# Performance work log

Measured on AMD Instinct MI355X. Metric: run time of the kernel, lower is better.

## Reference

```python
import jax, jax.numpy as jnp
import numpy as np

B, N, E, M, H, OUT, F = 4, 10000, 160000, 4, 64, 64, 64


def setup_inputs() -> dict:
    key = jax.random.key(0)
    k1, k2, k3, k4, k5, k6 = jax.random.split(key, 6)
    node_fts = jax.random.normal(k1, (B, N, M, H), dtype=jnp.float32)
    hidden = jax.random.normal(k2, (B, N, M, H), dtype=jnp.float32)
    edge_fts = jax.random.normal(k3, (B, E, F), dtype=jnp.float32)
    edge_indices = jax.random.randint(k4, (B, E, 2), 0, N, dtype=jnp.int64)
    # hk.Linear params (truncated-normal-ish init approximated by scaled normal)
    W_nh = jax.random.normal(k5, (2 * H, OUT), dtype=jnp.float32) / np.sqrt(2 * H)
    b_nh = jnp.zeros((OUT,), dtype=jnp.float32)
    W_e = jax.random.normal(k6, (F, 1), dtype=jnp.float32) / np.sqrt(F)
    b_e = jnp.zeros((1,), dtype=jnp.float32)
    return {"node_fts": node_fts, "hidden": hidden, "edge_fts": edge_fts,
            "W_nh": W_nh, "b_nh": b_nh, "W_e": W_e, "b_e": b_e,
            "edge_indices": edge_indices}


def reference(node_fts, hidden, edge_fts, W_nh, b_nh, W_e, b_e, edge_indices):
    nb_nodes = node_fts.shape[1]
    src = edge_indices[..., 0]  # [B, E]
    tgt = edge_indices[..., 1]  # [B, E]
    # fuse node and hidden features, project: [B, N, M, 2H] @ [2H, OUT]
    nh = jnp.concatenate([node_fts, hidden], axis=-1)
    nh_fts = jnp.einsum('bnmc,co->bnmo', nh, W_nh) + b_nh  # [B, N, M, OUT]
    # gather per-edge source-node features along node axis
    nh_values = jnp.take_along_axis(nh_fts, src[:, :, None, None], axis=1)  # [B, E, M, OUT]
    # scalar gate per edge
    edge_coeff = jnp.einsum('bef,fo->beo', edge_fts, W_e) + b_e  # [B, E, 1]
    filtered = edge_coeff[..., None] * nh_values  # [B, E, M, OUT]
    # scatter-sum messages to target nodes, per batch element
    seg = jax.vmap(lambda d, s: jax.ops.segment_sum(d, s, num_segments=nb_nodes))
    updated_bits = seg(filtered, tgt)  # [B, N, M, OUT]
    return updated_bits
```

## Files before the change

### kernel.cpp

```cpp
#include <hip/hip_runtime.h>

#define Bc 4
#define Nc 10000
#define Ec 160000
#define Mc 4
#define Hc 64
#define OUTc 64
#define Fc 64
#define ROWS (Bc * Nc * Mc)
#define TILES (ROWS / 16)
#define NSEG (Bc * Nc)
#define NEDGE (Bc * Ec)
#define PROJ_BLOCKS 2500
#define GATE_BLOCKS 2500
#define CAP 64

typedef __attribute__((ext_vector_type(8))) short bf16x8;
typedef __attribute__((ext_vector_type(4))) float f32x4;

__device__ __forceinline__ unsigned short f2bf(float f) {
    union { float f; unsigned u; } x; x.f = f;
    return (unsigned short)((x.u + 0x7FFFu + ((x.u >> 16) & 1u)) >> 16);
}
__device__ __forceinline__ float bfhi(unsigned u) {
    union { unsigned u; float f; } x; x.u = u & 0xFFFF0000u; return x.f;
}
__device__ __forceinline__ float bflo(unsigned u) {
    union { unsigned u; float f; } x; x.u = u << 16; return x.f;
}

__global__ __launch_bounds__(256) void proj_gate_kernel(
    const float* __restrict__ node, const float* __restrict__ hid,
    const float* __restrict__ Wnh, const float* __restrict__ bnh,
    unsigned short* __restrict__ nhf,
    const float* __restrict__ efts, const int* __restrict__ eidx,
    const float* __restrict__ We, const float* __restrict__ be,
    int2* __restrict__ epair, int* __restrict__ cnt)
{
    __shared__ __align__(16) unsigned short wlds[8192];
    const int lane = threadIdx.x & 63;

    if (blockIdx.x < PROJ_BLOCKS) {
        const int t = threadIdx.x;
#pragma unroll
        for (int i = 0; i < 4; ++i) {
            const int f    = t + 256 * i;
            const int kt   = f >> 8;
            const int ct   = (f >> 6) & 3;
            const int l    = f & 63;
            const int quad = l >> 4, m = l & 15;
            const int col  = 16 * ct + m;
            const int krow = quad * 8 + 32 * kt;
            bf16x8 fr;
#pragma unroll
            for (int j = 0; j < 8; ++j)
                fr[j] = (short)f2bf(Wnh[(size_t)(krow + j) * 64 + col]);
            *(bf16x8*)(wlds + (size_t)f * 8) = fr;
        }
        __syncthreads();

        const int tile = (int)(blockIdx.x * 4 + (threadIdx.x >> 6));
        const int m    = lane & 15;
        const int quad = lane >> 4;

        float bias[4];
#pragma unroll
        for (int ct = 0; ct < 4; ++ct) bias[ct] = bnh[m + 16 * ct];

        const int arow = tile * 16 + m;
        f32x4 acc[4];
#pragma unroll
        for (int ct = 0; ct < 4; ++ct) acc[ct] = (f32x4){0.f, 0.f, 0.f, 0.f};

#pragma unroll
        for (int kt = 0; kt < 4; ++kt) {
            const int kbase = quad * 8 + 32 * kt;
            const float* p = (kbase < 64)
                ? (node + (size_t)arow * 64 + kbase)
                : (hid  + (size_t)arow * 64 + (kbase - 64));
            const float4 lo = *(const float4*)p;
            const float4 hi = *(const float4*)(p + 4);
            bf16x8 a;
            a[0] = (short)f2bf(lo.x); a[1] = (short)f2bf(lo.y);
            a[2] = (short)f2bf(lo.z); a[3] = (short)f2bf(lo.w);
            a[4] = (short)f2bf(hi.x); a[5] = (short)f2bf(hi.y);
            a[6] = (short)f2bf(hi.z); a[7] = (short)f2bf(hi.w);
#pragma unroll
            for (int ct = 0; ct < 4; ++ct) {
                const bf16x8 bf = *(const bf16x8*)(wlds + (size_t)((kt * 4 + ct) * 64 + lane) * 8);
                acc[ct] = __builtin_amdgcn_mfma_f32_16x16x32_bf16(a, bf, acc[ct], 0, 0, 0);
            }
        }

        const int r0 = tile * 16 + quad * 4;
#pragma unroll
        for (int ct = 0; ct < 4; ++ct) {
            const int col = m + 16 * ct;
#pragma unroll
            for (int reg = 0; reg < 4; ++reg)
                nhf[(size_t)(r0 + reg) * 64 + col] = f2bf(acc[ct][reg] + bias[ct]);
        }
    } else {
        const int w  = (int)((blockIdx.x - PROJ_BLOCKS) * 4 + (threadIdx.x >> 6));
        const int e0 = w * 64;
        if (e0 >= NEDGE) return;
        const int b = e0 / Ec;

        const float4 w4 = *(const float4*)(We + (size_t)(lane & 15) * 4);
        const float* base = efts + (size_t)e0 * 64;
        float p[16];
#pragma unroll
        for (int j = 0; j < 16; ++j) {
            const float4 v = *(const float4*)(base + (size_t)j * 256 + lane * 4);
            p[j] = v.x * w4.x + v.y * w4.y + v.z * w4.z + v.w * w4.w;
        }
#pragma unroll
        for (int off = 1, n = 8; off < 16; off <<= 1, n >>= 1) {
            const bool hi = (lane & off) != 0;
#pragma unroll
            for (int i = 0; i < 8; ++i) {
                if (i < n) {
                    const float keep = hi ? p[2 * i + 1] : p[2 * i];
                    const float send = hi ? p[2 * i] : p[2 * i + 1];
                    p[i] = keep + __shfl_xor(send, off, 64);
                }
            }
        }
        const float c = p[0] + be[0];

        const int el = e0 + 4 * (lane & 15) + (lane >> 4);
        const int2 st = *(const int2*)(eidx + (size_t)el * 2);
        const int seg  = b * Nc + st.y;
        const int slot = atomicAdd(&cnt[seg], 1);
        if (slot < CAP)
            epair[(size_t)seg * 128 + slot] = make_int2(st.x, __float_as_int(c));
    }
}

__global__ __launch_bounds__(256) void gather_kernel(
    const int* __restrict__ cnt, const int2* epair,
    const unsigned* __restrict__ nhf, float* out)
{
    const int lane = threadIdx.x & 63;
    int seg = (int)((blockIdx.x * blockDim.x + threadIdx.x) >> 6);
    if (seg >= NSEG) return;
    seg = __builtin_amdgcn_readfirstlane(seg);
    const int b = seg / Nc;
    const int deg = cnt[seg];
    const int end = deg < CAP ? deg : CAP;
    const int2* bp = epair + (size_t)seg * 128;
    const unsigned* base = nhf + (size_t)b * Nc * 128 + lane * 2;

    f32x4 acc[4];
#pragma unroll
    for (int j = 0; j < 4; ++j) acc[j] = (f32x4){0.f, 0.f, 0.f, 0.f};

    int i = 0;
    for (; i + 8 <= end; i += 8) {
        int2 p[8]; uint2 r[8];
#pragma unroll
        for (int j = 0; j < 8; ++j) p[j] = bp[i + j];
#pragma unroll
        for (int j = 0; j < 8; ++j) r[j] = *(const uint2*)(base + (size_t)p[j].x * 128);
#pragma unroll
        for (int j = 0; j < 8; ++j) {
            const float c = __int_as_float(p[j].y);
            acc[j & 3][0] += c * bflo(r[j].x);
            acc[j & 3][1] += c * bfhi(r[j].x);
            acc[j & 3][2] += c * bflo(r[j].y);
            acc[j & 3][3] += c * bfhi(r[j].y);
        }
    }
    if (i + 4 <= end) {
        int2 p[4]; uint2 r[4];
#pragma unroll
        for (int j = 0; j < 4; ++j) p[j] = bp[i + j];
#pragma unroll
        for (int j = 0; j < 4; ++j) r[j] = *(const uint2*)(base + (size_t)p[j].x * 128);
#pragma unroll
        for (int j = 0; j < 4; ++j) {
            const float c = __int_as_float(p[j].y);
            acc[j][0] += c * bflo(r[j].x);
            acc[j][1] += c * bfhi(r[j].x);
            acc[j][2] += c * bflo(r[j].y);
            acc[j][3] += c * bfhi(r[j].y);
        }
        i += 4;
    }
    for (; i < end; ++i) {
        const int2 p = bp[i];
        const uint2 r = *(const uint2*)(base + (size_t)p.x * 128);
        const float c = __int_as_float(p.y);
        acc[0][0] += c * bflo(r.x);
        acc[0][1] += c * bfhi(r.x);
        acc[0][2] += c * bflo(r.y);
        acc[0][3] += c * bfhi(r.y);
    }
    float4 o;
    o.x = (acc[0][0] + acc[1][0]) + (acc[2][0] + acc[3][0]);
    o.y = (acc[0][1] + acc[1][1]) + (acc[2][1] + acc[3][1]);
    o.z = (acc[0][2] + acc[1][2]) + (acc[2][2] + acc[3][2]);
    o.w = (acc[0][3] + acc[1][3]) + (acc[2][3] + acc[3][3]);
    *(float4*)(out + (size_t)seg * 256 + lane * 4) = o;
}

__global__ __launch_bounds__(256) void edge_atomic_kernel(
    const float* __restrict__ efts, const int* __restrict__ eidx,
    const float* __restrict__ We, const float* __restrict__ be,
    const unsigned* __restrict__ nhf, float* __restrict__ out)
{
    const int lane = threadIdx.x & 63;
    const int eg   = (int)((blockIdx.x * blockDim.x + threadIdx.x) >> 6);
    if (eg >= NEDGE) return;
    const int b = eg / Ec;
    float c = efts[(size_t)eg * 64 + lane] * We[lane];
#pragma unroll
    for (int off = 32; off > 0; off >>= 1) c += __shfl_xor(c, off, 64);
    c += be[0];
    const int src = eidx[(size_t)eg * 2 + 0];
    const int tgt = eidx[(size_t)eg * 2 + 1];
    const uint2 r = *(const uint2*)(nhf + ((size_t)(b * Nc + src)) * 128 + lane * 2);
    float* op = out + ((size_t)(b * Nc + tgt)) * 256 + lane * 4;
    atomicAdd(op + 0, c * bflo(r.x));
    atomicAdd(op + 1, c * bfhi(r.x));
    atomicAdd(op + 2, c * bflo(r.y));
    atomicAdd(op + 3, c * bfhi(r.y));
}

extern "C" void kernel_launch(void* const* d_in, const int* in_sizes, int n_in,
                              void* d_out, int out_size, void* d_ws, size_t ws_size,
                              hipStream_t stream) {
    const float* node = (const float*)d_in[0];
    const float* hid  = (const float*)d_in[1];
    const float* efts = (const float*)d_in[2];
    const float* Wnh  = (const float*)d_in[3];
    const float* bnh  = (const float*)d_in[4];
    const float* We   = (const float*)d_in[5];
    const float* be   = (const float*)d_in[6];
    const int*   eidx = (const int*)d_in[7];
    float* out = (float*)d_out;

    unsigned* ws = (unsigned*)d_ws;
    unsigned short* nhf16 = (unsigned short*)ws;
    int* cnt = (int*)(ws + 5120000);
    const size_t ws_needed = (size_t)5160000 * 4;

    if (ws_size >= ws_needed) {
        int2* epair = (int2*)d_out;
        hipMemsetAsync(cnt, 0, (size_t)NSEG * sizeof(int), stream);
        proj_gate_kernel<<<PROJ_BLOCKS + GATE_BLOCKS, 256, 0, stream>>>(
            node, hid, Wnh, bnh, nhf16, efts, eidx, We, be, epair, cnt);
        gather_kernel<<<NSEG / 4, 256, 0, stream>>>(cnt, epair, (const unsigned*)ws, out);
    } else {
        proj_gate_kernel<<<PROJ_BLOCKS, 256, 0, stream>>>(
            node, hid, Wnh, bnh, nhf16, efts, eidx, We, be,
            (int2*)d_out , (int*)d_out );
        hipMemsetAsync(d_out, 0, (size_t)out_size * sizeof(float), stream);
        edge_atomic_kernel<<<NEDGE / 4, 256, 0, stream>>>(efts, eidx, We, be, (const unsigned*)ws, out);
    }
}
```

Measured before the change: 345.6 us.

## Split fused proj/gate kernel, double work per wave, broadcast edge pairs via shuffles

Splits the fused projection+gate kernel into separate proj and gate kernels. Each wave now handles two 16-row tiles (proj) or 128 edges (gate), with all loads issued before the math so memory latency overlaps compute. The gather kernel loads the segment's edge pairs once per lane and broadcasts them with shuffles instead of re-reading them from memory. The cost is an extra kernel launch, the loss of concurrency between projection and gate work, and higher register pressure.

Measured after the change: 351.9 us. About the same (+1.8%).

```diff
diff --git a/kernel.cpp b/kernel.cpp
--- a/kernel.cpp
+++ b/kernel.cpp
@@ -3,17 +3,11 @@
 #define Bc 4
 #define Nc 10000
 #define Ec 160000
-#define Mc 4
-#define Hc 64
-#define OUTc 64
-#define Fc 64
-#define ROWS (Bc * Nc * Mc)
-#define TILES (ROWS / 16)
 #define NSEG (Bc * Nc)
 #define NEDGE (Bc * Ec)
-#define PROJ_BLOCKS 2500
-#define GATE_BLOCKS 2500
 #define CAP 64
+#define PROJ_BLOCKS 1250
+#define GATE_BLOCKS 1250
 
 typedef __attribute__((ext_vector_type(8))) short bf16x8;
 typedef __attribute__((ext_vector_type(4))) float f32x4;
@@ -29,70 +23,89 @@
     union { unsigned u; float f; } x; x.u = u << 16; return x.f;
 }
 
-__global__ __launch_bounds__(256) void proj_gate_kernel(
+__device__ __forceinline__ float reduce16(float* p, int lane) {
+#pragma unroll
+    for (int off = 1, n = 8; off < 16; off <<= 1, n >>= 1) {
+        const bool hi2 = (lane & off) != 0;
+#pragma unroll
+        for (int i = 0; i < 8; ++i)
+            if (i < n) {
+                const float keep = hi2 ? p[2 * i + 1] : p[2 * i];
+                const float send = hi2 ? p[2 * i] : p[2 * i + 1];
+                p[i] = keep + __shfl_xor(send, off, 64);
+            }
+    }
+    return p[0];
+}
+
+__global__ __launch_bounds__(256) void proj_kernel(
     const float* __restrict__ node, const float* __restrict__ hid,
     const float* __restrict__ Wnh, const float* __restrict__ bnh,
-    unsigned short* __restrict__ nhf,
-    const float* __restrict__ efts, const int* __restrict__ eidx,
-    const float* __restrict__ We, const float* __restrict__ be,
-    int2* __restrict__ epair, int* __restrict__ cnt)
+    unsigned short* __restrict__ nhf)
 {
     __shared__ __align__(16) unsigned short wlds[8192];
-    const int lane = threadIdx.x & 63;
-
-    if (blockIdx.x < PROJ_BLOCKS) {
-        const int t = threadIdx.x;
-#pragma unroll
-        for (int i = 0; i < 4; ++i) {
-            const int f    = t + 256 * i;
-            const int kt   = f >> 8;
-            const int ct   = (f >> 6) & 3;
-            const int l    = f & 63;
-            const int quad = l >> 4, m = l & 15;
-            const int col  = 16 * ct + m;
-            const int krow = quad * 8 + 32 * kt;
-            bf16x8 fr;
-#pragma unroll
-            for (int j = 0; j < 8; ++j)
-                fr[j] = (short)f2bf(Wnh[(size_t)(krow + j) * 64 + col]);
-            *(bf16x8*)(wlds + (size_t)f * 8) = fr;
-        }
-        __syncthreads();
-
-        const int tile = (int)(blockIdx.x * 4 + (threadIdx.x >> 6));
-        const int m    = lane & 15;
-        const int quad = lane >> 4;
-
-        float bias[4];
-#pragma unroll
-        for (int ct = 0; ct < 4; ++ct) bias[ct] = bnh[m + 16 * ct];
-
-        const int arow = tile * 16 + m;
-        f32x4 acc[4];
-#pragma unroll
-        for (int ct = 0; ct < 4; ++ct) acc[ct] = (f32x4){0.f, 0.f, 0.f, 0.f};
-
+    const int t = threadIdx.x;
+    const int lane = t & 63;
+
+#pragma unroll
+    for (int i = 0; i < 4; ++i) {
+        const int f    = t + 256 * i;
+        const int kt   = f >> 8;
+        const int ct   = (f >> 6) & 3;
+        const int l    = f & 63;
+        const int quad = l >> 4, m = l & 15;
+        const int col  = 16 * ct + m;
+        const int krow = quad * 8 + 32 * kt;
+        bf16x8 fr;
+#pragma unroll
+        for (int j = 0; j < 8; ++j)
+            fr[j] = (short)f2bf(Wnh[(size_t)(krow + j) * 64 + col]);
+        *(bf16x8*)(wlds + (size_t)f * 8) = fr;
+    }
+    __syncthreads();
+
+    const int wv   = (int)(blockIdx.x * 4 + (t >> 6));
+    const int m    = lane & 15;
+    const int quad = lane >> 4;
+
+    float bias[4];
+#pragma unroll
+    for (int ct = 0; ct < 4; ++ct) bias[ct] = bnh[m + 16 * ct];
+
+    float4 lo[2][4], hi[2][4];
+#pragma unroll
+    for (int half = 0; half < 2; ++half) {
+        const int arow = (wv * 2 + half) * 16 + m;
 #pragma unroll
         for (int kt = 0; kt < 4; ++kt) {
             const int kbase = quad * 8 + 32 * kt;
-            const float* p = (kbase < 64)
+            const float* pp = (kbase < 64)
                 ? (node + (size_t)arow * 64 + kbase)
                 : (hid  + (size_t)arow * 64 + (kbase - 64));
-            const float4 lo = *(const float4*)p;
-            const float4 hi = *(const float4*)(p + 4);
+            lo[half][kt] = *(const float4*)pp;
+            hi[half][kt] = *(const float4*)(pp + 4);
+        }
+    }
+
+#pragma unroll
+    for (int half = 0; half < 2; ++half) {
+        f32x4 acc[4];
+#pragma unroll
+        for (int ct = 0; ct < 4; ++ct) acc[ct] = (f32x4){0.f, 0.f, 0.f, 0.f};
+#pragma unroll
+        for (int kt = 0; kt < 4; ++kt) {
             bf16x8 a;
-            a[0] = (short)f2bf(lo.x); a[1] = (short)f2bf(lo.y);
-            a[2] = (short)f2bf(lo.z); a[3] = (short)f2bf(lo.w);
-            a[4] = (short)f2bf(hi.x); a[5] = (short)f2bf(hi.y);
-            a[6] = (short)f2bf(hi.z); a[7] = (short)f2bf(hi.w);
+            a[0] = (short)f2bf(lo[half][kt].x); a[1] = (short)f2bf(lo[half][kt].y);
+            a[2] = (short)f2bf(lo[half][kt].z); a[3] = (short)f2bf(lo[half][kt].w);
+            a[4] = (short)f2bf(hi[half][kt].x); a[5] = (short)f2bf(hi[half][kt].y);
+            a[6] = (short)f2bf(hi[half][kt].z); a[7] = (short)f2bf(hi[half][kt].w);
 #pragma unroll
             for (int ct = 0; ct < 4; ++ct) {
                 const bf16x8 bf = *(const bf16x8*)(wlds + (size_t)((kt * 4 + ct) * 64 + lane) * 8);
                 acc[ct] = __builtin_amdgcn_mfma_f32_16x16x32_bf16(a, bf, acc[ct], 0, 0, 0);
             }
         }
-
-        const int r0 = tile * 16 + quad * 4;
+        const int r0 = (wv * 2 + half) * 16 + quad * 4;
 #pragma unroll
         for (int ct = 0; ct < 4; ++ct) {
             const int col = m + 16 * ct;
@@ -100,40 +113,59 @@
             for (int reg = 0; reg < 4; ++reg)
                 nhf[(size_t)(r0 + reg) * 64 + col] = f2bf(acc[ct][reg] + bias[ct]);
         }
-    } else {
-        const int w  = (int)((blockIdx.x - PROJ_BLOCKS) * 4 + (threadIdx.x >> 6));
-        const int e0 = w * 64;
-        if (e0 >= NEDGE) return;
-        const int b = e0 / Ec;
-
-        const float4 w4 = *(const float4*)(We + (size_t)(lane & 15) * 4);
-        const float* base = efts + (size_t)e0 * 64;
-        float p[16];
-#pragma unroll
-        for (int j = 0; j < 16; ++j) {
-            const float4 v = *(const float4*)(base + (size_t)j * 256 + lane * 4);
-            p[j] = v.x * w4.x + v.y * w4.y + v.z * w4.z + v.w * w4.w;
-        }
-#pragma unroll
-        for (int off = 1, n = 8; off < 16; off <<= 1, n >>= 1) {
-            const bool hi = (lane & off) != 0;
-#pragma unroll
-            for (int i = 0; i < 8; ++i) {
-                if (i < n) {
-                    const float keep = hi ? p[2 * i + 1] : p[2 * i];
-                    const float send = hi ? p[2 * i] : p[2 * i + 1];
-                    p[i] = keep + __shfl_xor(send, off, 64);
-                }
-            }
-        }
-        const float c = p[0] + be[0];
-
-        const int el = e0 + 4 * (lane & 15) + (lane >> 4);
-        const int2 st = *(const int2*)(eidx + (size_t)el * 2);
-        const int seg  = b * Nc + st.y;
+    }
+}
+
+__global__ __launch_bounds__(256) void gate_kernel(
+    const float* __restrict__ efts, const int* __restrict__ eidx,
+    const float* __restrict__ We, const float* __restrict__ be,
+    int2* __restrict__ epair, int* __restrict__ cnt)
+{
+    const int lane = threadIdx.x & 63;
+    const int w  = (int)(blockIdx.x * 4 + (threadIdx.x >> 6));
+    const int e0 = w * 128;
+    const int b  = e0 / Ec;
+    const int cb = b * Nc;
+    const float4 w4 = *(const float4*)(We + (size_t)(lane & 15) * 4);
+    const float be0 = be[0];
+    const int perm = 4 * (lane & 15) + (lane >> 4);
+
+    float4 v[16];
+    const float* base0 = efts + (size_t)e0 * 64;
+#pragma unroll
+    for (int j = 0; j < 16; ++j)
+        v[j] = *(const float4*)(base0 + (size_t)j * 256 + lane * 4);
+    const int2 st0 = *(const int2*)(eidx + (size_t)(e0 + perm) * 2);
+
+    float p[16];
+#pragma unroll
+    for (int j = 0; j < 16; ++j)
+        p[j] = v[j].x * w4.x + v[j].y * w4.y + v[j].z * w4.z + v[j].w * w4.w;
+
+    const float* base1 = efts + (size_t)(e0 + 64) * 64;
+#pragma unroll
+    for (int j = 0; j < 16; ++j)
+        v[j] = *(const float4*)(base1 + (size_t)j * 256 + lane * 4);
+    const int2 st1 = *(const int2*)(eidx + (size_t)(e0 + 64 + perm) * 2);
+
+    {
+        const float cval = reduce16(p, lane) + be0;
+        const int seg  = cb + st0.y;
         const int slot = atomicAdd(&cnt[seg], 1);
         if (slot < CAP)
-            epair[(size_t)seg * 128 + slot] = make_int2(st.x, __float_as_int(c));
+            epair[(size_t)seg * 128 + slot] = make_int2(st0.x, __float_as_int(cval));
+    }
+
+#pragma unroll
+    for (int j = 0; j < 16; ++j)
+        p[j] = v[j].x * w4.x + v[j].y * w4.y + v[j].z * w4.z + v[j].w * w4.w;
+
+    {
+        const float cval = reduce16(p, lane) + be0;
+        const int seg  = cb + st1.y;
+        const int slot = atomicAdd(&cnt[seg], 1);
+        if (slot < CAP)
+            epair[(size_t)seg * 128 + slot] = make_int2(st1.x, __float_as_int(cval));
     }
 }
 
@@ -150,6 +182,7 @@
     const int end = deg < CAP ? deg : CAP;
     const int2* bp = epair + (size_t)seg * 128;
     const unsigned* base = nhf + (size_t)b * Nc * 128 + lane * 2;
+    const int2 my = bp[lane];
 
     f32x4 acc[4];
 #pragma unroll
@@ -157,44 +190,48 @@
 
     int i = 0;
     for (; i + 8 <= end; i += 8) {
-        int2 p[8]; uint2 r[8];
-#pragma unroll
-        for (int j = 0; j < 8; ++j) p[j] = bp[i + j];
-#pragma unroll
-        for (int j = 0; j < 8; ++j) r[j] = *(const uint2*)(base + (size_t)p[j].x * 128);
+        int sx[8]; float cc[8]; uint2 r[8];
 #pragma unroll
         for (int j = 0; j < 8; ++j) {
-            const float c = __int_as_float(p[j].y);
-            acc[j & 3][0] += c * bflo(r[j].x);
-            acc[j & 3][1] += c * bfhi(r[j].x);
-            acc[j & 3][2] += c * bflo(r[j].y);
-            acc[j & 3][3] += c * bfhi(r[j].y);
+            sx[j] = __shfl(my.x, i + j, 64);
+            cc[j] = __int_as_float(__shfl(my.y, i + j, 64));
+        }
+#pragma unroll
+        for (int j = 0; j < 8; ++j) r[j] = *(const uint2*)(base + (size_t)sx[j] * 128);
+#pragma unroll
+        for (int j = 0; j < 8; ++j) {
+            acc[j & 3][0] += cc[j] * bflo(r[j].x);
+            acc[j & 3][1] += cc[j] * bfhi(r[j].x);
+            acc[j & 3][2] += cc[j] * bflo(r[j].y);
+            acc[j & 3][3] += cc[j] * bfhi(r[j].y);
         }
     }
     if (i + 4 <= end) {
-        int2 p[4]; uint2 r[4];
-#pragma unroll
-        for (int j = 0; j < 4; ++j) p[j] = bp[i + j];
-#pragma unroll
-        for (int j = 0; j < 4; ++j) r[j] = *(const uint2*)(base + (size_t)p[j].x * 128);
+        int sx[4]; float cc[4]; uint2 r[4];
 #pragma unroll
         for (int j = 0; j < 4; ++j) {
-            const float c = __int_as_float(p[j].y);
-            acc[j][0] += c * bflo(r[j].x);
-            acc[j][1] += c * bfhi(r[j].x);
-            acc[j][2] += c * bflo(r[j].y);
-            acc[j][3] += c * bfhi(r[j].y);
+            sx[j] = __shfl(my.x, i + j, 64);
+            cc[j] = __int_as_float(__shfl(my.y, i + j, 64));
+        }
+#pragma unroll
+        for (int j = 0; j < 4; ++j) r[j] = *(const uint2*)(base + (size_t)sx[j] * 128);
+#pragma unroll
+        for (int j = 0; j < 4; ++j) {
+            acc[j][0] += cc[j] * bflo(r[j].x);
+            acc[j][1] += cc[j] * bfhi(r[j].x);
+            acc[j][2] += cc[j] * bflo(r[j].y);
+            acc[j][3] += cc[j] * bfhi(r[j].y);
         }
         i += 4;
     }
     for (; i < end; ++i) {
-        const int2 p = bp[i];
-        const uint2 r = *(const uint2*)(base + (size_t)p.x * 128);
-        const float c = __int_as_float(p.y);
-        acc[0][0] += c * bflo(r.x);
-        acc[0][1] += c * bfhi(r.x);
-        acc[0][2] += c * bflo(r.y);
-        acc[0][3] += c * bfhi(r.y);
+        const int sx = __shfl(my.x, i, 64);
+        const float cc = __int_as_float(__shfl(my.y, i, 64));
+        const uint2 r = *(const uint2*)(base + (size_t)sx * 128);
+        acc[0][0] += cc * bflo(r.x);
+        acc[0][1] += cc * bfhi(r.x);
+        acc[0][2] += cc * bflo(r.y);
+        acc[0][3] += cc * bfhi(r.y);
     }
     float4 o;
     o.x = (acc[0][0] + acc[1][0]) + (acc[2][0] + acc[3][0]);
@@ -248,13 +285,11 @@
     if (ws_size >= ws_needed) {
         int2* epair = (int2*)d_out;
         hipMemsetAsync(cnt, 0, (size_t)NSEG * sizeof(int), stream);
-        proj_gate_kernel<<<PROJ_BLOCKS + GATE_BLOCKS, 256, 0, stream>>>(
-            node, hid, Wnh, bnh, nhf16, efts, eidx, We, be, epair, cnt);
+        proj_kernel<<<PROJ_BLOCKS, 256, 0, stream>>>(node, hid, Wnh, bnh, nhf16);
+        gate_kernel<<<GATE_BLOCKS, 256, 0, stream>>>(efts, eidx, We, be, epair, cnt);
         gather_kernel<<<NSEG / 4, 256, 0, stream>>>(cnt, epair, (const unsigned*)ws, out);
     } else {
-        proj_gate_kernel<<<PROJ_BLOCKS, 256, 0, stream>>>(
-            node, hid, Wnh, bnh, nhf16, efts, eidx, We, be,
-            (int2*)d_out , (int*)d_out );
+        proj_kernel<<<PROJ_BLOCKS, 256, 0, stream>>>(node, hid, Wnh, bnh, nhf16);
         hipMemsetAsync(d_out, 0, (size_t)out_size * sizeof(float), stream);
         edge_atomic_kernel<<<NEDGE / 4, 256, 0, stream>>>(efts, eidx, We, be, (const unsigned*)ws, out);
     }
```
